# Performance work log

Hardware: AMD Instinct MI355X
Metric: run time of the kernel (lower is better)

Reference implementation:

```python
import jax, jax.numpy as jnp
import numpy as np

NUM_EXPERTS = 8
TOP_K = 2
ROUTED_SCALE = 1.0  # routed_scaling_factor
D_MODEL = 2048
D_FFN = 1408


def setup_inputs() -> dict:
    key = jax.random.key(0)
    ks = jax.random.split(key, 8)
    s = 0.02  # init scale for weights
    return {
        'hidden_states': jax.random.normal(ks[0], (2, 1024, D_MODEL), jnp.float32),
        'gate_w': jax.random.normal(ks[1], (NUM_EXPERTS, D_MODEL), jnp.float32) * s,
        'w_gate': jax.random.normal(ks[2], (NUM_EXPERTS, D_MODEL, D_FFN), jnp.float32) * s,
        'w_up': jax.random.normal(ks[3], (NUM_EXPERTS, D_MODEL, D_FFN), jnp.float32) * s,
        'w_down': jax.random.normal(ks[4], (NUM_EXPERTS, D_FFN, D_MODEL), jnp.float32) * s,
        'sw_gate': jax.random.normal(ks[5], (D_MODEL, D_FFN), jnp.float32) * s,
        'sw_up': jax.random.normal(ks[6], (D_MODEL, D_FFN), jnp.float32) * s,
        'sw_down': jax.random.normal(ks[7], (D_FFN, D_MODEL), jnp.float32) * s,
    }


def reference(hidden_states, gate_w, w_gate, w_up, w_down, sw_gate, sw_up, sw_down):
    B, S, D = hidden_states.shape
    x = hidden_states.reshape(-1, D)            # [T, D]
    T = x.shape[0]

    # --- router: fp32 linear -> softmax -> top-k -> renormalize ---
    logits = jnp.einsum('td,ed->te', x.astype(jnp.float32), gate_w)   # [T, E]
    probs = jax.nn.softmax(logits, axis=-1)
    topk_w, topk_ids = jax.lax.top_k(probs, TOP_K)                    # [T, K]
    topk_w = topk_w / jnp.sum(topk_w, axis=-1, keepdims=True)         # norm_topk_prob
    # dense per-token expert gates [T, E] (zero for unselected experts)
    gates = jnp.zeros((T, NUM_EXPERTS), jnp.float32).at[
        jnp.arange(T)[:, None], topk_ids].add(topk_w)
    gates = gates.astype(x.dtype)

    # --- routed experts: SwiGLU per expert, masked dense combine ---
    g = jnp.einsum('td,edf->etf', x, w_gate)    # [E, T, F]
    u = jnp.einsum('td,edf->etf', x, w_up)      # [E, T, F]
    h = jax.nn.silu(g) * u                      # SiluAndMul
    down = jnp.einsum('etf,efd->etd', h, w_down)  # [E, T, D]
    routed = jnp.einsum('te,etd->td', gates, down)  # combine
    routed = routed * ROUTED_SCALE

    # --- shared expert MLP ---
    shared = (jax.nn.silu(x @ sw_gate) * (x @ sw_up)) @ sw_down

    out = routed + shared
    return out.reshape(B, S, D)
```

## Files before the change

### kernel.cpp

```cpp
#include <hip/hip_runtime.h>
#include <hip/hip_bf16.h>

#define T_TOK 2048
#define DM    2048
#define FF    1408
#define NE    8
#define MT_ROUTED 40
#define MT_TOTAL  56
#define ROUTED_CAP 5120
#define NSLOT 7168

typedef unsigned short u16;
typedef __attribute__((ext_vector_type(4))) u16 u16x4;
typedef __attribute__((ext_vector_type(8))) short bf16x8;
typedef __attribute__((ext_vector_type(4))) float f32x4;

__device__ __forceinline__ u16 f2bf(float f) {
    unsigned u = __float_as_uint(f);
    unsigned r = (u + 0x7FFFu + ((u >> 16) & 1u)) >> 16;
    return (u16)r;
}
__device__ __forceinline__ float bf2f(u16 v) {
    return __uint_as_float(((unsigned)v) << 16);
}

__device__ __forceinline__ void gll16(const void* g, void* l) {
    __builtin_amdgcn_global_load_lds((const __attribute__((address_space(1))) void*)g,
                                     (__attribute__((address_space(3))) void*)l, 16, 0, 0);
}

constexpr size_t SZ_XB  = (size_t)T_TOK * DM * 2;
constexpr size_t SZ_WE  = (size_t)NE * DM * FF * 2;
constexpr size_t SZ_SW  = (size_t)DM * FF * 2;
constexpr size_t SZ_H   = (size_t)NSLOT * FF * 2;
constexpr size_t SZ_DN  = (size_t)NSLOT * DM * 2;

constexpr size_t OFF_XB   = 0;
constexpr size_t OFF_WGT  = OFF_XB + SZ_XB;
constexpr size_t OFF_WUT  = OFF_WGT + SZ_WE;
constexpr size_t OFF_WDT  = OFF_WUT + SZ_WE;
constexpr size_t OFF_SWG  = OFF_WDT + SZ_WE;
constexpr size_t OFF_SWU  = OFF_SWG + SZ_SW;
constexpr size_t OFF_SWD  = OFF_SWU + SZ_SW;
constexpr size_t OFF_H    = OFF_SWD + SZ_SW;
constexpr size_t OFF_DN   = OFF_H + SZ_H;
constexpr size_t OFF_TID  = OFF_DN + SZ_DN;
constexpr size_t OFF_TW   = OFF_TID + (size_t)T_TOK*2*4;
constexpr size_t OFF_PERM = OFF_TW  + (size_t)T_TOK*2*4;
constexpr size_t OFF_SW_S = OFF_PERM + (size_t)ROUTED_CAP*4;
constexpr size_t OFF_TKS  = OFF_SW_S + (size_t)ROUTED_CAP*4;
constexpr size_t OFF_TE   = OFF_TKS + (size_t)T_TOK*2*4;

__global__ void tcvt_kernel(const float* __restrict__ wg, const float* __restrict__ wu,
                            const float* __restrict__ swg, const float* __restrict__ swu,
                            const float* __restrict__ wd, const float* __restrict__ swd,
                            u16* __restrict__ wgT, u16* __restrict__ wuT,
                            u16* __restrict__ swgT, u16* __restrict__ swuT,
                            u16* __restrict__ wdT, u16* __restrict__ swdT) {
    __shared__ u16 tile[64][72];
    const int z = blockIdx.z;
    const size_t msz = (size_t)DM * FF;
    const float* s; u16* d; int R, C, trow, tcol;
    if (z < 18) {
        R = DM; C = FF;
        trow = blockIdx.x / 22; tcol = blockIdx.x % 22;
        if (z < 8)       { s = wg + (size_t)z * msz;       d = wgT + (size_t)z * msz; }
        else if (z < 16) { s = wu + (size_t)(z - 8) * msz; d = wuT + (size_t)(z - 8) * msz; }
        else if (z == 16){ s = swg;                         d = swgT; }
        else             { s = swu;                         d = swuT; }
    } else {
        R = FF; C = DM;
        trow = blockIdx.x / 32; tcol = blockIdx.x % 32;
        if (z < 26) { s = wd + (size_t)(z - 18) * msz; d = wdT + (size_t)(z - 18) * msz; }
        else        { s = swd;                          d = swdT; }
    }
    const int r0 = trow * 64, c0 = tcol * 64;
    const int tr = threadIdx.x >> 4, tc = (threadIdx.x & 15) * 4;
#pragma unroll
    for (int i = 0; i < 4; i++) {
        const int r = tr + i * 16;
        const float4 v = *(const float4*)(s + (size_t)(r0 + r) * C + (c0 + tc));
        tile[r][tc+0] = f2bf(v.x); tile[r][tc+1] = f2bf(v.y);
        tile[r][tc+2] = f2bf(v.z); tile[r][tc+3] = f2bf(v.w);
    }
    __syncthreads();
#pragma unroll
    for (int i = 0; i < 4; i++) {
        const int c = tr + i * 16;
        u16x4 o;
        o.x = tile[tc+0][c]; o.y = tile[tc+1][c]; o.z = tile[tc+2][c]; o.w = tile[tc+3][c];
        *(u16x4*)(d + (size_t)(c0 + c) * R + (r0 + tc)) = o;
    }
}

__global__ void router_kernel(const float* __restrict__ x, const float* __restrict__ gw,
                              u16* __restrict__ xb,
                              int* __restrict__ topk_id, float* __restrict__ topk_w) {
    const int wv = threadIdx.x >> 6, l = threadIdx.x & 63;
    const int t = blockIdx.x * 4 + wv;
    const float* xt = x + (size_t)t * DM;
    u16* xbt = xb + (size_t)t * DM;
    float acc[NE] = {0.f,0.f,0.f,0.f,0.f,0.f,0.f,0.f};
    for (int d = l * 4; d < DM; d += 256) {
        const float4 xv = *(const float4*)(xt + d);
        u16x4 o; o.x = f2bf(xv.x); o.y = f2bf(xv.y); o.z = f2bf(xv.z); o.w = f2bf(xv.w);
        *(u16x4*)(xbt + d) = o;
#pragma unroll
        for (int e = 0; e < NE; e++) {
            const float4 w4 = *(const float4*)(gw + e * DM + d);
            acc[e] += xv.x * w4.x + xv.y * w4.y + xv.z * w4.z + xv.w * w4.w;
        }
    }
#pragma unroll
    for (int e = 0; e < NE; e++)
#pragma unroll
        for (int off = 32; off > 0; off >>= 1) acc[e] += __shfl_xor(acc[e], off, 64);
    if (l == 0) {
        float m = acc[0];
#pragma unroll
        for (int e = 1; e < NE; e++) m = fmaxf(m, acc[e]);
        float p[NE];
#pragma unroll
        for (int e = 0; e < NE; e++) p[e] = __expf(acc[e] - m);
        int i1 = 0; float b1 = p[0];
#pragma unroll
        for (int e = 1; e < NE; e++) if (p[e] > b1) { b1 = p[e]; i1 = e; }
        int i2 = -1; float b2 = -1.f;
#pragma unroll
        for (int e = 0; e < NE; e++) if (e != i1 && p[e] > b2) { b2 = p[e]; i2 = e; }
        const float s = b1 + b2;
        topk_id[2*t] = i1; topk_id[2*t+1] = i2;
        topk_w[2*t] = b1 / s; topk_w[2*t+1] = b2 / s;
    }
}

__global__ void scan_kernel(const int* __restrict__ topk_id, const float* __restrict__ topk_w,
                            int* __restrict__ perm_token, float* __restrict__ slot_w,
                            int* __restrict__ tk_slot, int* __restrict__ tile_e) {
    const int e = blockIdx.x;
    const int tid = threadIdx.x;
    __shared__ int cnt[NE];
    __shared__ int tsum[256];
    int ids[16];
#pragma unroll
    for (int j = 0; j < 16; j++) ids[j] = topk_id[tid * 16 + j];
    if (tid < NE) cnt[tid] = 0;
    __syncthreads();
#pragma unroll
    for (int e2 = 0; e2 < NE; e2++) {
        int c = 0;
#pragma unroll
        for (int j = 0; j < 16; j++) c += (ids[j] == e2);
        if (c) atomicAdd(&cnt[e2], c);
    }
    int mySum = 0;
#pragma unroll
    for (int j = 0; j < 16; j++) mySum += (ids[j] == e);
    tsum[tid] = mySum;
    __syncthreads();
    if (tid == 0) { int run = 0; for (int i = 0; i < 256; i++) { int v = tsum[i]; tsum[i] = run; run += v; } }
    __syncthreads();
    int poff = 0;
#pragma unroll
    for (int e2 = 0; e2 < NE; e2++) { int p = (cnt[e2] + 127) & ~127; if (e2 < e) poff += p; }
    const int padded_e = (cnt[e] + 127) & ~127;
    int run = tsum[tid];
#pragma unroll
    for (int j = 0; j < 16; j++) {
        if (ids[j] == e) {
            const int i = tid * 16 + j;
            const int slot = poff + run;
            perm_token[slot] = i >> 1;
            slot_w[slot] = topk_w[i];
            tk_slot[i] = slot;
            run++;
        }
    }
    for (int r = cnt[e] + tid; r < padded_e; r += 256) { perm_token[poff + r] = 0; slot_w[poff + r] = 0.f; }
    if (tid == 0) for (int tt = poff >> 7; tt < (poff + padded_e) >> 7; tt++) tile_e[tt] = e;
    if (e == 0 && tid == 1) {
        int ptot = 0;
#pragma unroll
        for (int e2 = 0; e2 < NE; e2++) ptot += (cnt[e2] + 127) & ~127;
        for (int tt = ptot >> 7; tt < MT_ROUTED; tt++) tile_e[tt] = -1;
        for (int tt = MT_ROUTED; tt < MT_TOTAL; tt++) tile_e[tt] = 8;
    }
}

__global__ __launch_bounds__(256, 2)
void gemm1_kernel(const u16* __restrict__ xb,
                  const u16* __restrict__ wgT, const u16* __restrict__ wuT,
                  const u16* __restrict__ swgT, const u16* __restrict__ swuT,
                  const int* __restrict__ perm_token, const float* __restrict__ slot_w,
                  const int* __restrict__ tile_e, u16* __restrict__ hbuf) {
    const int bid = blockIdx.x;
    const int swz = (bid & 7) * 154 + (bid >> 3);
    const int mtile = swz % 56, ntile = swz / 56;
    const int e = tile_e[mtile];
    if (e < 0) return;
    __shared__ u16 lA[2][128 * 64], lB[2][128 * 64];
    __shared__ int lTok[128];
    __shared__ float lW[128];
    const int tid = threadIdx.x, l = tid & 63, w = tid >> 6;
    const bool sh = (e == 8);
    const int slot_base = sh ? (ROUTED_CAP + (mtile - MT_ROUTED) * 128) : mtile * 128;
    if (tid < 128) {
        if (sh) { lTok[tid] = (mtile - MT_ROUTED) * 128 + tid; lW[tid] = 1.0f; }
        else    { lTok[tid] = perm_token[slot_base + tid]; lW[tid] = slot_w[slot_base + tid]; }
    }
    __syncthreads();
    const u16* Bg = sh ? swgT : (wgT + (size_t)e * FF * DM);
    const u16* Bu = sh ? swuT : (wuT + (size_t)e * FF * DM);
    const int n0 = ntile * 64;
    const u16* aSrc[4]; const u16* bSrc[4]; int ldsOff[4];
#pragma unroll
    for (int i = 0; i < 4; i++) {
        const int row = i * 32 + w * 8 + (l >> 3);
        const int ch = (l & 7) ^ (row & 7);
        ldsOff[i] = (i * 32 + w * 8) * 64;
        aSrc[i] = xb + (size_t)lTok[row] * DM + ch * 8;
        const u16* bbase = (i < 2) ? (Bg + (size_t)(n0 + row) * DM)
                                   : (Bu + (size_t)(n0 + row - 64) * DM);
        bSrc[i] = bbase + ch * 8;
    }
    f32x4 acc[2][8] = {};
    const int wm = w * 32;

    auto stage = [&](int buf, int k0) {
#pragma unroll
        for (int i = 0; i < 4; i++) {
            gll16(aSrc[i] + k0, lA[buf] + ldsOff[i]);
            gll16(bSrc[i] + k0, lB[buf] + ldsOff[i]);
        }
    };
    auto compute = [&](int buf) {
#pragma unroll
        for (int kk = 0; kk < 64; kk += 32) {
            bf16x8 af[2], bf_[8];
#pragma unroll
            for (int mi = 0; mi < 2; mi++) {
                const int row = wm + mi * 16 + (l & 15);
                const int ch = ((kk >> 3) + (l >> 4)) ^ (row & 7);
                af[mi] = *(const bf16x8*)(lA[buf] + row * 64 + ch * 8);
            }
#pragma unroll
            for (int ni = 0; ni < 8; ni++) {
                const int row = ni * 16 + (l & 15);
                const int ch = ((kk >> 3) + (l >> 4)) ^ (row & 7);
                bf_[ni] = *(const bf16x8*)(lB[buf] + row * 64 + ch * 8);
            }
#pragma unroll
            for (int mi = 0; mi < 2; mi++)
#pragma unroll
                for (int ni = 0; ni < 8; ni++)
                    acc[mi][ni] = __builtin_amdgcn_mfma_f32_16x16x32_bf16(af[mi], bf_[ni], acc[mi][ni], 0, 0, 0);
        }
    };

    stage(0, 0);
    for (int t = 0; t < 31; t++) {
        const int cur = t & 1;
        stage(cur ^ 1, (t + 1) * 64);
        asm volatile("s_waitcnt vmcnt(8)" ::: "memory");
        __builtin_amdgcn_s_barrier();
        compute(cur);
        __builtin_amdgcn_s_barrier();
    }
    asm volatile("s_waitcnt vmcnt(0)" ::: "memory");
    __builtin_amdgcn_s_barrier();
    compute(1);

#pragma unroll
    for (int mi = 0; mi < 2; mi++)
#pragma unroll
        for (int r = 0; r < 4; r++) {
            const int m = wm + mi * 16 + (l >> 4) * 4 + r;
            const float wgt = lW[m];
#pragma unroll
            for (int ni = 0; ni < 4; ni++) {
                const int n = ni * 16 + (l & 15);
                const float g = acc[mi][ni][r], u = acc[mi][ni + 4][r];
                const float h = g * (1.f / (1.f + __expf(-g))) * u * wgt;
                hbuf[(size_t)(slot_base + m) * FF + n0 + n] = f2bf(h);
            }
        }
}

__global__ __launch_bounds__(256, 3)
void gemm2_kernel(const u16* __restrict__ hbuf, const u16* __restrict__ wdT,
                  const u16* __restrict__ swdT, const int* __restrict__ tile_e,
                  u16* __restrict__ dn) {
    const int bid = blockIdx.x;
    const int swz = (bid & 7) * 224 + (bid >> 3);
    const int mtile = swz % 56, ntile = swz / 56;
    const int e = tile_e[mtile];
    if (e < 0) return;
    __shared__ u16 lA[2][128 * 64], lB[2][64 * 64];
    const int tid = threadIdx.x, l = tid & 63, w = tid >> 6;
    const bool sh = (e == 8);
    const int slot_base = sh ? (ROUTED_CAP + (mtile - MT_ROUTED) * 128) : mtile * 128;
    const u16* Bp = sh ? swdT : (wdT + (size_t)e * DM * FF);
    const int n0 = ntile * 64;
    const u16* aSrc[4]; const u16* bSrc[2]; int aOff[4], bOff[2];
#pragma unroll
    for (int i = 0; i < 4; i++) {
        const int row = i * 32 + w * 8 + (l >> 3);
        const int ch = (l & 7) ^ (row & 7);
        aOff[i] = (i * 32 + w * 8) * 64;
        aSrc[i] = hbuf + (size_t)(slot_base + row) * FF + ch * 8;
    }
#pragma unroll
    for (int i = 0; i < 2; i++) {
        const int row = i * 32 + w * 8 + (l >> 3);
        const int ch = (l & 7) ^ (row & 7);
        bOff[i] = (i * 32 + w * 8) * 64;
        bSrc[i] = Bp + (size_t)(n0 + row) * FF + ch * 8;
    }
    f32x4 acc[2][4] = {};
    const int wm = w * 32;

    auto stage = [&](int buf, int k0) {
#pragma unroll
        for (int i = 0; i < 4; i++) gll16(aSrc[i] + k0, lA[buf] + aOff[i]);
#pragma unroll
        for (int i = 0; i < 2; i++) gll16(bSrc[i] + k0, lB[buf] + bOff[i]);
    };
    auto compute = [&](int buf) {
#pragma unroll
        for (int kk = 0; kk < 64; kk += 32) {
            bf16x8 af[2], bf_[4];
#pragma unroll
            for (int mi = 0; mi < 2; mi++) {
                const int row = wm + mi * 16 + (l & 15);
                const int ch = ((kk >> 3) + (l >> 4)) ^ (row & 7);
                af[mi] = *(const bf16x8*)(lA[buf] + row * 64 + ch * 8);
            }
#pragma unroll
            for (int ni = 0; ni < 4; ni++) {
                const int row = ni * 16 + (l & 15);
                const int ch = ((kk >> 3) + (l >> 4)) ^ (row & 7);
                bf_[ni] = *(const bf16x8*)(lB[buf] + row * 64 + ch * 8);
            }
#pragma unroll
            for (int mi = 0; mi < 2; mi++)
#pragma unroll
                for (int ni = 0; ni < 4; ni++)
                    acc[mi][ni] = __builtin_amdgcn_mfma_f32_16x16x32_bf16(af[mi], bf_[ni], acc[mi][ni], 0, 0, 0);
        }
    };

    stage(0, 0);
    for (int t = 0; t < 21; t++) {
        const int cur = t & 1;
        stage(cur ^ 1, (t + 1) * 64);
        asm volatile("s_waitcnt vmcnt(6)" ::: "memory");
        __builtin_amdgcn_s_barrier();
        compute(cur);
        __builtin_amdgcn_s_barrier();
    }
    asm volatile("s_waitcnt vmcnt(0)" ::: "memory");
    __builtin_amdgcn_s_barrier();
    compute(1);

#pragma unroll
    for (int mi = 0; mi < 2; mi++)
#pragma unroll
        for (int r = 0; r < 4; r++) {
            const int m = wm + mi * 16 + (l >> 4) * 4 + r;
#pragma unroll
            for (int ni = 0; ni < 4; ni++) {
                const int n = ni * 16 + (l & 15);
                dn[(size_t)(slot_base + m) * DM + n0 + n] = f2bf(acc[mi][ni][r]);
            }
        }
}

__global__ void combine_kernel(const u16* __restrict__ dn, const int* __restrict__ tk_slot,
                               float* __restrict__ out) {
    const int i = blockIdx.x * 256 + threadIdx.x;
    const int base = i * 8;
    const int t = base >> 11, d = base & 2047;
    const int s1 = tk_slot[2 * t], s2 = tk_slot[2 * t + 1];
    const bf16x8 a = *(const bf16x8*)(dn + (size_t)s1 * DM + d);
    const bf16x8 b = *(const bf16x8*)(dn + (size_t)s2 * DM + d);
    const bf16x8 c = *(const bf16x8*)(dn + (size_t)(ROUTED_CAP + t) * DM + d);
    float o[8];
#pragma unroll
    for (int j = 0; j < 8; j++)
        o[j] = bf2f((u16)a[j]) + bf2f((u16)b[j]) + bf2f((u16)c[j]);
    float4 lo, hi;
    lo.x = o[0]; lo.y = o[1]; lo.z = o[2]; lo.w = o[3];
    hi.x = o[4]; hi.y = o[5]; hi.z = o[6]; hi.w = o[7];
    *(float4*)(out + base) = lo;
    *(float4*)(out + base + 4) = hi;
}

extern "C" void kernel_launch(void* const* d_in, const int* in_sizes, int n_in,
                              void* d_out, int out_size, void* d_ws, size_t ws_size,
                              hipStream_t stream) {
    (void)in_sizes; (void)n_in; (void)out_size; (void)ws_size;
    const float* x   = (const float*)d_in[0];
    const float* gw  = (const float*)d_in[1];
    const float* wg  = (const float*)d_in[2];
    const float* wu  = (const float*)d_in[3];
    const float* wd  = (const float*)d_in[4];
    const float* swg = (const float*)d_in[5];
    const float* swu = (const float*)d_in[6];
    const float* swd = (const float*)d_in[7];
    float* out = (float*)d_out;
    char* ws = (char*)d_ws;

    u16*   xb    = (u16*)(ws + OFF_XB);
    u16*   wgT   = (u16*)(ws + OFF_WGT);
    u16*   wuT   = (u16*)(ws + OFF_WUT);
    u16*   wdT   = (u16*)(ws + OFF_WDT);
    u16*   swgT  = (u16*)(ws + OFF_SWG);
    u16*   swuT  = (u16*)(ws + OFF_SWU);
    u16*   swdT  = (u16*)(ws + OFF_SWD);
    u16*   hbuf  = (u16*)(ws + OFF_H);
    u16*   dn    = (u16*)(ws + OFF_DN);
    int*   tid_  = (int*)(ws + OFF_TID);
    float* tw    = (float*)(ws + OFF_TW);
    int*   perm  = (int*)(ws + OFF_PERM);
    float* slw   = (float*)(ws + OFF_SW_S);
    int*   tks   = (int*)(ws + OFF_TKS);
    int*   te    = (int*)(ws + OFF_TE);

    router_kernel<<<T_TOK / 4, 256, 0, stream>>>(x, gw, xb, tid_, tw);
    scan_kernel<<<NE, 256, 0, stream>>>(tid_, tw, perm, slw, tks, te);
    tcvt_kernel<<<dim3(704, 1, 27), 256, 0, stream>>>(wg, wu, swg, swu, wd, swd,
                                                      wgT, wuT, swgT, swuT, wdT, swdT);
    gemm1_kernel<<<1232, 256, 0, stream>>>(xb, wgT, wuT, swgT, swuT, perm, slw, te, hbuf);
    gemm2_kernel<<<1792, 256, 0, stream>>>(hbuf, wdT, swdT, te, dn);
    combine_kernel<<<(T_TOK * DM / 8) / 256, 256, 0, stream>>>(dn, tks, out);
}
```

Baseline: 343.7 us.

## Drop LDS double buffering in GEMM kernels to raise occupancy

Both expert GEMM kernels move from a double-buffered LDS pipeline with explicit vmcnt waits to a single LDS buffer with __syncthreads before and after each K-step load. This halves shared memory per block, and the launch bounds are raised (gemm1 2→4, gemm2 3→5) so more blocks can be resident per CU. The intent is to hide memory latency by running more concurrent blocks instead of prefetching within a block. The cost is that each block now stalls on every global load with no overlap, and the higher occupancy target may force register spills.

```diff
diff --git a/kernel.cpp b/kernel.cpp
--- a/kernel.cpp
+++ b/kernel.cpp
@@ -187,7 +187,7 @@
     }
 }
 
-__global__ __launch_bounds__(256, 2)
+__global__ __launch_bounds__(256, 4)
 void gemm1_kernel(const u16* __restrict__ xb,
                   const u16* __restrict__ wgT, const u16* __restrict__ wuT,
                   const u16* __restrict__ swgT, const u16* __restrict__ swuT,
@@ -198,7 +198,7 @@
     const int mtile = swz % 56, ntile = swz / 56;
     const int e = tile_e[mtile];
     if (e < 0) return;
-    __shared__ u16 lA[2][128 * 64], lB[2][128 * 64];
+    __shared__ u16 lA[128 * 64], lB[128 * 64];
     __shared__ int lTok[128];
     __shared__ float lW[128];
     const int tid = threadIdx.x, l = tid & 63, w = tid >> 6;
@@ -225,15 +225,11 @@
     }
     f32x4 acc[2][8] = {};
     const int wm = w * 32;
-
-    auto stage = [&](int buf, int k0) {
-#pragma unroll
-        for (int i = 0; i < 4; i++) {
-            gll16(aSrc[i] + k0, lA[buf] + ldsOff[i]);
-            gll16(bSrc[i] + k0, lB[buf] + ldsOff[i]);
-        }
-    };
-    auto compute = [&](int buf) {
+    for (int k0 = 0; k0 < DM; k0 += 64) {
+        __syncthreads();
+#pragma unroll
+        for (int i = 0; i < 4; i++) { gll16(aSrc[i] + k0, lA + ldsOff[i]); gll16(bSrc[i] + k0, lB + ldsOff[i]); }
+        __syncthreads();
 #pragma unroll
         for (int kk = 0; kk < 64; kk += 32) {
             bf16x8 af[2], bf_[8];
@@ -241,13 +237,13 @@
             for (int mi = 0; mi < 2; mi++) {
                 const int row = wm + mi * 16 + (l & 15);
                 const int ch = ((kk >> 3) + (l >> 4)) ^ (row & 7);
-                af[mi] = *(const bf16x8*)(lA[buf] + row * 64 + ch * 8);
+                af[mi] = *(const bf16x8*)(lA + row * 64 + ch * 8);
             }
 #pragma unroll
             for (int ni = 0; ni < 8; ni++) {
                 const int row = ni * 16 + (l & 15);
                 const int ch = ((kk >> 3) + (l >> 4)) ^ (row & 7);
-                bf_[ni] = *(const bf16x8*)(lB[buf] + row * 64 + ch * 8);
+                bf_[ni] = *(const bf16x8*)(lB + row * 64 + ch * 8);
             }
 #pragma unroll
             for (int mi = 0; mi < 2; mi++)
@@ -255,21 +251,7 @@
                 for (int ni = 0; ni < 8; ni++)
                     acc[mi][ni] = __builtin_amdgcn_mfma_f32_16x16x32_bf16(af[mi], bf_[ni], acc[mi][ni], 0, 0, 0);
         }
-    };
-
-    stage(0, 0);
-    for (int t = 0; t < 31; t++) {
-        const int cur = t & 1;
-        stage(cur ^ 1, (t + 1) * 64);
-        asm volatile("s_waitcnt vmcnt(8)" ::: "memory");
-        __builtin_amdgcn_s_barrier();
-        compute(cur);
-        __builtin_amdgcn_s_barrier();
-    }
-    asm volatile("s_waitcnt vmcnt(0)" ::: "memory");
-    __builtin_amdgcn_s_barrier();
-    compute(1);
-
+    }
 #pragma unroll
     for (int mi = 0; mi < 2; mi++)
 #pragma unroll
@@ -286,7 +268,7 @@
         }
 }
 
-__global__ __launch_bounds__(256, 3)
+__global__ __launch_bounds__(256, 5)
 void gemm2_kernel(const u16* __restrict__ hbuf, const u16* __restrict__ wdT,
                   const u16* __restrict__ swdT, const int* __restrict__ tile_e,
                   u16* __restrict__ dn) {
@@ -295,7 +277,7 @@
     const int mtile = swz % 56, ntile = swz / 56;
     const int e = tile_e[mtile];
     if (e < 0) return;
-    __shared__ u16 lA[2][128 * 64], lB[2][64 * 64];
+    __shared__ u16 lA[128 * 64], lB[64 * 64];
     const int tid = threadIdx.x, l = tid & 63, w = tid >> 6;
     const bool sh = (e == 8);
     const int slot_base = sh ? (ROUTED_CAP + (mtile - MT_ROUTED) * 128) : mtile * 128;
@@ -318,14 +300,13 @@
     }
     f32x4 acc[2][4] = {};
     const int wm = w * 32;
-
-    auto stage = [&](int buf, int k0) {
-#pragma unroll
-        for (int i = 0; i < 4; i++) gll16(aSrc[i] + k0, lA[buf] + aOff[i]);
-#pragma unroll
-        for (int i = 0; i < 2; i++) gll16(bSrc[i] + k0, lB[buf] + bOff[i]);
-    };
-    auto compute = [&](int buf) {
+    for (int k0 = 0; k0 < FF; k0 += 64) {
+        __syncthreads();
+#pragma unroll
+        for (int i = 0; i < 4; i++) gll16(aSrc[i] + k0, lA + aOff[i]);
+#pragma unroll
+        for (int i = 0; i < 2; i++) gll16(bSrc[i] + k0, lB + bOff[i]);
+        __syncthreads();
 #pragma unroll
         for (int kk = 0; kk < 64; kk += 32) {
             bf16x8 af[2], bf_[4];
@@ -333,13 +314,13 @@
             for (int mi = 0; mi < 2; mi++) {
                 const int row = wm + mi * 16 + (l & 15);
                 const int ch = ((kk >> 3) + (l >> 4)) ^ (row & 7);
-                af[mi] = *(const bf16x8*)(lA[buf] + row * 64 + ch * 8);
+                af[mi] = *(const bf16x8*)(lA + row * 64 + ch * 8);
             }
 #pragma unroll
             for (int ni = 0; ni < 4; ni++) {
                 const int row = ni * 16 + (l & 15);
                 const int ch = ((kk >> 3) + (l >> 4)) ^ (row & 7);
-                bf_[ni] = *(const bf16x8*)(lB[buf] + row * 64 + ch * 8);
+                bf_[ni] = *(const bf16x8*)(lB + row * 64 + ch * 8);
             }
 #pragma unroll
             for (int mi = 0; mi < 2; mi++)
@@ -347,21 +328,7 @@
                 for (int ni = 0; ni < 4; ni++)
                     acc[mi][ni] = __builtin_amdgcn_mfma_f32_16x16x32_bf16(af[mi], bf_[ni], acc[mi][ni], 0, 0, 0);
         }
-    };
-
-    stage(0, 0);
-    for (int t = 0; t < 21; t++) {
-        const int cur = t & 1;
-        stage(cur ^ 1, (t + 1) * 64);
-        asm volatile("s_waitcnt vmcnt(6)" ::: "memory");
-        __builtin_amdgcn_s_barrier();
-        compute(cur);
-        __builtin_amdgcn_s_barrier();
-    }
-    asm volatile("s_waitcnt vmcnt(0)" ::: "memory");
-    __builtin_amdgcn_s_barrier();
-    compute(1);
-
+    }
 #pragma unroll
     for (int mi = 0; mi < 2; mi++)
 #pragma unroll
```

Measured after the change: 321.7 us. 6.4% less time.
